# Kernel tuning notes

Measured on AMD Instinct MI355X. Metric: run time of the kernel, lower is better.

## Reference

```python
import jax, jax.numpy as jnp
import numpy as np

TAU = 2.0      # spikingjelly LIFNode tau
V_TH = 1.0     # default v_threshold
ALPHA = 2.0    # default ATan surrogate alpha
T_STEPS = 32   # output_size (repeat count along time)

# Heaviside spike with ATan surrogate gradient (spikingjelly surrogate.ATan)
@jax.custom_vjp
def spike_fn(x):
    return (x >= 0.0).astype(x.dtype)

def _spike_fwd(x):
    return spike_fn(x), x

def _spike_bwd(x, g):
    sg = (ALPHA / 2.0) / (1.0 + (jnp.pi / 2.0 * ALPHA * x) ** 2)
    return (g * sg,)

spike_fn.defvjp(_spike_fwd, _spike_bwd)


def setup_inputs() -> dict:
    key = jax.random.key(0)
    inputs = jax.random.normal(key, (64, 64, 512), dtype=jnp.float32)  # [B, C, L]
    return {"inputs": inputs}


def reference(inputs):
    # repeat([T,1,1,1]) then permute(0,1,3,2): every step sees the same [B,L,C] frame
    xt = jnp.transpose(inputs, (0, 2, 1))  # [B, L, C]
    v0 = jnp.zeros_like(xt)                # v_reset = 0.0 initial membrane

    def step(v, _):
        # LIF with decay_input=True, hard reset to v_reset=0:
        # v = v + (x - (v - v_reset)) / tau
        v = v + (xt - v) / TAU
        s = spike_fn(v - V_TH)
        # hard reset; detach_reset=True -> spike detached in reset path
        v = v * (1.0 - jax.lax.stop_gradient(s))
        return v, s

    _, spks = jax.lax.scan(step, v0, None, length=T_STEPS)  # [T, B, L, C]
    return jnp.transpose(spks, (1, 0, 2, 3))                # [B, T, L, C]
```

## Files before the change

kernel.cpp:

```cpp
#include <hip/hip_runtime.h>


constexpr int B = 64;
constexpr int C = 64;
constexpr int L = 512;
constexpr int T = 32;

__global__ __launch_bounds__(256) void lif_repeat_kernel(
    const float* __restrict__ in, float* __restrict__ out) {
  const int g = blockIdx.x * blockDim.x + threadIdx.x;
  const int c4 = g & 15;
  const int l  = (g >> 4) & 511;
  const int b  = g >> 13;
  const int c  = c4 * 4;

  const float* ip = in + (size_t)b * (C * L) + (size_t)c * L + l;
  const float x0 = ip[0 * L];
  const float x1 = ip[1 * L];
  const float x2 = ip[2 * L];
  const float x3 = ip[3 * L];

  float4* op = (float4*)(out + (size_t)b * (T * L * C) + (size_t)l * C + c);
  constexpr int t_stride4 = (L * C) / 4;

  float v0 = 0.f, v1 = 0.f, v2 = 0.f, v3 = 0.f;
#pragma unroll
  for (int t = 0; t < T; ++t) {
    v0 += (x0 - v0) * 0.5f;
    v1 += (x1 - v1) * 0.5f;
    v2 += (x2 - v2) * 0.5f;
    v3 += (x3 - v3) * 0.5f;
    const float s0 = (v0 >= 1.0f) ? 1.0f : 0.0f;
    const float s1 = (v1 >= 1.0f) ? 1.0f : 0.0f;
    const float s2 = (v2 >= 1.0f) ? 1.0f : 0.0f;
    const float s3 = (v3 >= 1.0f) ? 1.0f : 0.0f;
    op[(size_t)t * t_stride4] = make_float4(s0, s1, s2, s3);
    v0 = (s0 != 0.0f) ? 0.0f : v0;
    v1 = (s1 != 0.0f) ? 0.0f : v1;
    v2 = (s2 != 0.0f) ? 0.0f : v2;
    v3 = (s3 != 0.0f) ? 0.0f : v3;
  }
}

extern "C" void kernel_launch(void* const* d_in, const int* in_sizes, int n_in,
                              void* d_out, int out_size, void* d_ws, size_t ws_size,
                              hipStream_t stream) {
  const float* in = (const float*)d_in[0];
  float* out = (float*)d_out;
  const int n_threads = (B * L * C) / 4;
  const int block = 256;
  const int grid = n_threads / block;
  lif_repeat_kernel<<<grid, block, 0, stream>>>(in, out);
}
```

Baseline: 264.8 us.

## Stage input transpose through LDS and use nontemporal output stores

Each block now loads a 64-channel by 16-position tile of the input with coalesced float4 reads, transposes it through shared memory, and then each thread reads its four channels from LDS. This replaces the strided per-thread global reads of the old version. The output spike stores become nontemporal, which avoids polluting the cache with the large write-only output. In exchange the kernel adds a barrier and LDS traffic, and the LDS writes may hit bank conflicts.

```diff
diff --git a/kernel.cpp b/kernel.cpp
--- a/kernel.cpp
+++ b/kernel.cpp
@@ -6,39 +6,52 @@
 constexpr int L = 512;
 constexpr int T = 32;
 
+typedef float vf4 __attribute__((ext_vector_type(4)));
+
 __global__ __launch_bounds__(256) void lif_repeat_kernel(
     const float* __restrict__ in, float* __restrict__ out) {
-  const int g = blockIdx.x * blockDim.x + threadIdx.x;
-  const int c4 = g & 15;
-  const int l  = (g >> 4) & 511;
-  const int b  = g >> 13;
-  const int c  = c4 * 4;
+  __shared__ float lds[16 * 64];
+  const int blk = blockIdx.x;
+  const int tid = threadIdx.x;
+  const int b  = blk >> 5;
+  const int l0 = (blk & 31) * 16;
 
-  const float* ip = in + (size_t)b * (C * L) + (size_t)c * L + l;
-  const float x0 = ip[0 * L];
-  const float x1 = ip[1 * L];
-  const float x2 = ip[2 * L];
-  const float x3 = ip[3 * L];
+  {
+    const int c = tid >> 2;
+    const int q = tid & 3;
+    const vf4 v = *(const vf4*)(in + (size_t)b * (C * L) + (size_t)c * L + l0 + q * 4);
+    float* p = lds + c;
+    p[(q * 4 + 0) * 64] = v.x;
+    p[(q * 4 + 1) * 64] = v.y;
+    p[(q * 4 + 2) * 64] = v.z;
+    p[(q * 4 + 3) * 64] = v.w;
+  }
+  __syncthreads();
 
-  float4* op = (float4*)(out + (size_t)b * (T * L * C) + (size_t)l * C + c);
+  const int c4 = tid & 15;
+  const int ll = tid >> 4;
+  const vf4 x = *(const vf4*)(lds + ll * 64 + c4 * 4);
+
+  vf4* op = (vf4*)(out + (size_t)b * (T * L * C) + (size_t)(l0 + ll) * C + c4 * 4);
   constexpr int t_stride4 = (L * C) / 4;
 
   float v0 = 0.f, v1 = 0.f, v2 = 0.f, v3 = 0.f;
 #pragma unroll
   for (int t = 0; t < T; ++t) {
-    v0 += (x0 - v0) * 0.5f;
-    v1 += (x1 - v1) * 0.5f;
-    v2 += (x2 - v2) * 0.5f;
-    v3 += (x3 - v3) * 0.5f;
-    const float s0 = (v0 >= 1.0f) ? 1.0f : 0.0f;
-    const float s1 = (v1 >= 1.0f) ? 1.0f : 0.0f;
-    const float s2 = (v2 >= 1.0f) ? 1.0f : 0.0f;
-    const float s3 = (v3 >= 1.0f) ? 1.0f : 0.0f;
-    op[(size_t)t * t_stride4] = make_float4(s0, s1, s2, s3);
-    v0 = (s0 != 0.0f) ? 0.0f : v0;
-    v1 = (s1 != 0.0f) ? 0.0f : v1;
-    v2 = (s2 != 0.0f) ? 0.0f : v2;
-    v3 = (s3 != 0.0f) ? 0.0f : v3;
+    v0 += (x.x - v0) * 0.5f;
+    v1 += (x.y - v1) * 0.5f;
+    v2 += (x.z - v2) * 0.5f;
+    v3 += (x.w - v3) * 0.5f;
+    vf4 s;
+    s.x = (v0 >= 1.0f) ? 1.0f : 0.0f;
+    s.y = (v1 >= 1.0f) ? 1.0f : 0.0f;
+    s.z = (v2 >= 1.0f) ? 1.0f : 0.0f;
+    s.w = (v3 >= 1.0f) ? 1.0f : 0.0f;
+    __builtin_nontemporal_store(s, op + (size_t)t * t_stride4);
+    v0 = (s.x != 0.0f) ? 0.0f : v0;
+    v1 = (s.y != 0.0f) ? 0.0f : v1;
+    v2 = (s.z != 0.0f) ? 0.0f : v2;
+    v3 = (s.w != 0.0f) ? 0.0f : v3;
   }
 }
 
@@ -47,8 +60,6 @@
                               hipStream_t stream) {
   const float* in = (const float*)d_in[0];
   float* out = (float*)d_out;
-  const int n_threads = (B * L * C) / 4;
-  const int block = 256;
-  const int grid = n_threads / block;
-  lif_repeat_kernel<<<grid, block, 0, stream>>>(in, out);
+  const int grid = B * 32;
+  lif_repeat_kernel<<<grid, 256, 0, stream>>>(in, out);
 }
```

Result: slower. 272.5 us (+2.9%).
